# Kernel tuning notes

Hardware: AMD Instinct MI355X
Metric: run time of the kernel (lower is better)

Reference implementation:

```python
import jax, jax.numpy as jnp
import numpy as np
import math

HIDDEN = 1024
HEADS = 16
HEAD_DIM = HIDDEN // HEADS
B, S = 4, 4096


def setup_inputs() -> dict:
    key = jax.random.key(0)
    ks = jax.random.split(key, 9)
    std = 1.0 / math.sqrt(HIDDEN)
    mk = lambda k: (jax.random.normal(k, (HIDDEN, HIDDEN), jnp.float32) * std)
    return {
        "x": jax.random.normal(ks[0], (B, S, HIDDEN), jnp.float32),
        "Wq": mk(ks[1]), "bq": jnp.zeros((HIDDEN,), jnp.float32),
        "Wk": mk(ks[2]), "bk": jnp.zeros((HIDDEN,), jnp.float32),
        "Wv": mk(ks[3]), "bv": jnp.zeros((HIDDEN,), jnp.float32),
        "Wo": mk(ks[4]), "bo": jnp.zeros((HIDDEN,), jnp.float32),
    }


def reference(x, Wq, bq, Wk, bk, Wv, bv, Wo, bo):
    b, s, _ = x.shape
    scale = 1.0 / math.sqrt(HEAD_DIM)
    # projections: [b, s, hidden] -> [b, heads, s, head_dim]
    def proj(W, bias):
        y = jnp.einsum('bsh,hd->bsd', x, W.T) + bias  # torch Linear: x @ W.T + b
        return y.reshape(b, s, HEADS, HEAD_DIM).transpose(0, 2, 1, 3)
    q = proj(Wq, bq)
    k = proj(Wk, bk)
    v = proj(Wv, bv)
    # FFT along sequence axis (axis=2)
    q_f = jnp.fft.rfft(q, axis=2)
    k_f = jnp.fft.rfft(k, axis=2)
    v_f = jnp.fft.rfft(v, axis=2)
    out_f = q_f * jnp.conj(k_f) * v_f
    out = jnp.fft.irfft(out_f, n=s, axis=2) * scale
    out = out.transpose(0, 2, 1, 3).reshape(b, s, HIDDEN)
    out = jnp.einsum('bsh,hd->bsd', out, Wo.T) + bo
    # dropout is identity in eval mode
    return out
```

## Files before the change

### kernel.cpp

```cpp
#include <hip/hip_runtime.h>
#include <hip/hip_bf16.h>
#include <math.h>

#define HIDDEN   1024
#define HEADS    16
#define HEAD_DIM 64
#define BATCH    4
#define SEQ      4096
#define M_TOTAL  (BATCH * SEQ)
#define FFT_N    4096
#define WSZ      ((size_t)HIDDEN * HIDDEN)
#define PI2      6.28318530717958647692f

typedef _Float16 f16x8 __attribute__((ext_vector_type(8)));
typedef float    f32x4 __attribute__((ext_vector_type(4)));

#if defined(__has_builtin)
#if __has_builtin(__builtin_amdgcn_global_load_lds)
#define HAVE_GLL 1
#else
#define HAVE_GLL 0
#endif
#else
#define HAVE_GLL 0
#endif

#if HAVE_GLL
__device__ __forceinline__ void gload16(const void* g, void* l) {
    __builtin_amdgcn_global_load_lds(
        (const __attribute__((address_space(1))) unsigned int*)g,
        (__attribute__((address_space(3))) unsigned int*)l,
        16, 0, 0);
}
#endif

__device__ __forceinline__ void cvt8_f16(float4 v0, float4 v1,
                                         ushort* __restrict__ d) {
    const float vv[8] = {v0.x, v0.y, v0.z, v0.w, v1.x, v1.y, v1.z, v1.w};
    f16x8 hv;
    #pragma unroll
    for (int e = 0; e < 8; ++e) hv[e] = (_Float16)vv[e];
    *(f16x8*)d = hv;
}

__global__ __launch_bounds__(256) void cvt16_kernel(
    const float* __restrict__ src, ushort* __restrict__ h)
{
    const size_t i = ((size_t)blockIdx.x * 256 + threadIdx.x) * 8;
    float4 v0 = *(const float4*)(src + i);
    float4 v1 = *(const float4*)(src + i + 4);
    cvt8_f16(v0, v1, h + i);
}

__global__ __launch_bounds__(256) void cvtW_kernel(
    const float* __restrict__ Wq, const float* __restrict__ Wk,
    const float* __restrict__ Wv, const float* __restrict__ Wo,
    ushort* __restrict__ wh, ushort* __restrict__ woh)
{
    const int p = blockIdx.y;
    const size_t i = ((size_t)blockIdx.x * 256 + threadIdx.x) * 8;
    const float* __restrict__ src = (p == 0) ? Wq : (p == 1 ? Wk : (p == 2 ? Wv : Wo));
    ushort* __restrict__ dst = (p < 3) ? (wh + (size_t)p * WSZ) : woh;
    float4 v0 = *(const float4*)(src + i);
    float4 v1 = *(const float4*)(src + i + 4);
    cvt8_f16(v0, v1, dst + i);
}

__global__ __launch_bounds__(1024, 1) void gemm_qkv_mfma8(
    const ushort* __restrict__ xh, const ushort* __restrict__ wh,
    const float* __restrict__ bq, const float* __restrict__ bk,
    const float* __restrict__ bv,
    ushort* __restrict__ qkvt)
{
    __shared__ ushort Ah[3][8192];
    __shared__ ushort Bh[3][8192];

    const int tid  = threadIdx.x;
    const int lane = tid & 63;
    const int wid  = tid >> 6;
    const int wr   = wid >> 2;
    const int wc   = wid & 3;
    const int m0   = blockIdx.x * 256;
    const int ng0  = blockIdx.y * 256;
    const int p    = ng0 >> 10;
    const int n0p  = ng0 & 1023;

    const float* __restrict__ bias = (p == 0) ? bq : (p == 1 ? bk : bv);
    ushort* __restrict__ ct = qkvt + (size_t)p * HIDDEN * M_TOTAL;

    const int row = tid >> 2;
    const int chS = (tid & 3) ^ ((row >> 1) & 3);

    const int fr = lane & 15;
    const int fc = lane >> 4;
    const int cc = (fc ^ ((fr >> 1) & 3)) * 8;

    f32x4 acc[4][4];
    #pragma unroll
    for (int rf = 0; rf < 4; ++rf)
        #pragma unroll
        for (int cf = 0; cf < 4; ++cf)
            acc[rf][cf] = (f32x4){0.f, 0.f, 0.f, 0.f};

#if HAVE_GLL
    #define QKV_STAGE(K0, SLOT) {                                                  \
        const size_t gw = (size_t)(ng0 + row) * HIDDEN + (K0) + (size_t)chS * 8;   \
        const size_t gx = (size_t)(m0 + row) * HIDDEN + (K0) + (size_t)chS * 8;    \
        gload16(wh + gw, &Ah[SLOT][(size_t)tid * 8]);                              \
        gload16(xh + gx, &Bh[SLOT][(size_t)tid * 8]);                              \
    }
#else
    #define QKV_STAGE(K0, SLOT) {                                                  \
        const size_t gw = (size_t)(ng0 + row) * HIDDEN + (K0) + (size_t)chS * 8;   \
        const size_t gx = (size_t)(m0 + row) * HIDDEN + (K0) + (size_t)chS * 8;    \
        *(f16x8*)&Ah[SLOT][(size_t)tid * 8] = *(const f16x8*)(wh + gw);            \
        *(f16x8*)&Bh[SLOT][(size_t)tid * 8] = *(const f16x8*)(xh + gx);            \
    }
#endif

    QKV_STAGE(0, 0);
    QKV_STAGE(32, 1);

    for (int ks = 0; ks < 32; ++ks) {
        const int slot = ks % 3;
#if HAVE_GLL
        if (ks == 31) { asm volatile("s_waitcnt vmcnt(0)" ::: "memory"); }
        else          { asm volatile("s_waitcnt vmcnt(2)" ::: "memory"); }
        __builtin_amdgcn_s_barrier();
        asm volatile("" ::: "memory");
#else
        __syncthreads();
#endif
        {
            const ushort* pAh = Ah[slot];
            const ushort* pBh = Bh[slot];
            f16x8 a_h[4], b_h[4];
            #pragma unroll
            for (int rf = 0; rf < 4; ++rf) {
                const int R = wr * 64 + rf * 16 + fr;
                a_h[rf] = *(const f16x8*)(pAh + R * 32 + cc);
            }
            #pragma unroll
            for (int cf = 0; cf < 4; ++cf) {
                const int R = wc * 64 + cf * 16 + fr;
                b_h[cf] = *(const f16x8*)(pBh + R * 32 + cc);
            }
            #pragma unroll
            for (int rf = 0; rf < 4; ++rf)
                #pragma unroll
                for (int cf = 0; cf < 4; ++cf)
                    acc[rf][cf] = __builtin_amdgcn_mfma_f32_16x16x32_f16(a_h[rf], b_h[cf], acc[rf][cf], 0, 0, 0);
        }
        if (ks + 2 < 32) { QKV_STAGE((ks + 2) * 32, (ks + 2) % 3); }
#if !HAVE_GLL
        __syncthreads();
#endif
    }
    #undef QKV_STAGE

    const int rq = lane >> 4;
    #pragma unroll
    for (int rf = 0; rf < 4; ++rf) {
        #pragma unroll
        for (int r = 0; r < 4; ++r) {
            const int nl = wr * 64 + rf * 16 + rq * 4 + r;
            const float bv = bias[n0p + nl];
            ushort* dst = ct + (size_t)(n0p + nl) * M_TOTAL + m0 + wc * 64;
            #pragma unroll
            for (int cf = 0; cf < 4; ++cf) {
                union { _Float16 f; ushort u; } cvt;
                cvt.f = (_Float16)(acc[rf][cf][r] + bv);
                dst[cf * 16 + fr] = cvt.u;
            }
        }
    }
}

__device__ __forceinline__ float2 cmul(float2 a, float2 b) {
    return {a.x*b.x - a.y*b.y, a.x*b.y + a.y*b.x};
}

__device__ __forceinline__ int phys(int p) { return p ^ ((p >> 4) & 15); }

template<int DIR>
__device__ __forceinline__ void dft16(const float2* x, float2* X) {
    float2 t[16];
    #pragma unroll
    for (int n0 = 0; n0 < 4; ++n0) {
        float2 a = x[n0], b = x[n0+4], c = x[n0+8], d = x[n0+12];
        float2 s0 = {a.x+c.x, a.y+c.y}, s1 = {a.x-c.x, a.y-c.y};
        float2 s2 = {b.x+d.x, b.y+d.y}, s3 = {b.x-d.x, b.y-d.y};
        t[n0*4+0] = {s0.x+s2.x, s0.y+s2.y};
        t[n0*4+2] = {s0.x-s2.x, s0.y-s2.y};
        if (DIR < 0) {
            t[n0*4+1] = {s1.x+s3.y, s1.y-s3.x};
            t[n0*4+3] = {s1.x-s3.y, s1.y+s3.x};
        } else {
            t[n0*4+1] = {s1.x-s3.y, s1.y+s3.x};
            t[n0*4+3] = {s1.x+s3.y, s1.y-s3.x};
        }
    }
    const float C1 = 0.92387953251128674f;
    const float S1_ = 0.38268343236508978f;
    const float R2 = 0.70710678118654752f;
    #define TW(idx, cc_, ss_) t[idx] = cmul(t[idx], (float2){cc_, DIR*(ss_)})
    TW(1*4+1, C1, S1_);   TW(1*4+2, R2, R2);    TW(1*4+3, S1_, C1);
    TW(2*4+1, R2, R2);    TW(2*4+2, 0.f, 1.f);  TW(2*4+3, -R2, R2);
    TW(3*4+1, S1_, C1);   TW(3*4+2, -R2, R2);   TW(3*4+3, -C1, -S1_);
    #undef TW
    #pragma unroll
    for (int k0 = 0; k0 < 4; ++k0) {
        float2 a = t[0+k0], b = t[4+k0], c = t[8+k0], d = t[12+k0];
        float2 s0 = {a.x+c.x, a.y+c.y}, s1 = {a.x-c.x, a.y-c.y};
        float2 s2 = {b.x+d.x, b.y+d.y}, s3 = {b.x-d.x, b.y-d.y};
        X[k0+0]  = {s0.x+s2.x, s0.y+s2.y};
        X[k0+8]  = {s0.x-s2.x, s0.y-s2.y};
        if (DIR < 0) {
            X[k0+4]  = {s1.x+s3.y, s1.y-s3.x};
            X[k0+12] = {s1.x-s3.y, s1.y+s3.x};
        } else {
            X[k0+4]  = {s1.x-s3.y, s1.y+s3.x};
            X[k0+12] = {s1.x+s3.y, s1.y-s3.x};
        }
    }
}

__device__ __forceinline__ void twiddle_apply(float2* y, float ang) {
    float s, c;
    __sincosf(ang, &s, &c);
    const float2 base = {c, s};
    float2 w = base;
    #pragma unroll
    for (int u = 1; u < 16; ++u) {
        y[u] = cmul(y[u], w);
        w = cmul(w, base);
    }
}

__global__ __launch_bounds__(256) void fft_attn_kernel(
    const ushort* __restrict__ qt, const ushort* __restrict__ kt,
    const ushort* __restrict__ vt, float* __restrict__ ot)
{
    __shared__ float2 bufA[FFT_N];
    __shared__ float2 bufB[FFT_N];

    const int tid = threadIdx.x;
    const int bid = blockIdx.x;
    const int n   = bid >> 2;
    const int b   = bid & 3;

    const size_t off = (size_t)n * M_TOTAL + (size_t)b * SEQ;
    const _Float16* qrow = (const _Float16*)qt + off;
    const _Float16* krow = (const _Float16*)kt + off;
    const _Float16* vrow = (const _Float16*)vt + off;
    float*          orow = ot + off;

    {
        const int q = tid;
        float2 xA[16], xB[16], yA[16], yB[16];
        #pragma unroll
        for (int r = 0; r < 16; ++r) {
            xA[r] = { (float)qrow[q + 256*r], (float)krow[q + 256*r] };
            xB[r] = { (float)vrow[q + 256*r], 0.f };
        }
        dft16<-1>(xA, yA);
        dft16<-1>(xB, yB);
        const float ang = -PI2 * (float)q / 4096.f;
        twiddle_apply(yA, ang);
        twiddle_apply(yB, ang);
        #pragma unroll
        for (int u = 0; u < 16; ++u) {
            bufA[phys(q + 256*u)] = yA[u];
            bufB[phys(q + 256*u)] = yB[u];
        }
    }
    __syncthreads();
    {
        const int blk = tid >> 4, a = tid & 15;
        const int base = 256*blk + a;
        float2 xA[16], xB[16], yA[16], yB[16];
        #pragma unroll
        for (int c = 0; c < 16; ++c) {
            xA[c] = bufA[phys(base + 16*c)];
            xB[c] = bufB[phys(base + 16*c)];
        }
        dft16<-1>(xA, yA);
        dft16<-1>(xB, yB);
        const float ang = -PI2 * (float)a / 256.f;
        twiddle_apply(yA, ang);
        twiddle_apply(yB, ang);
        #pragma unroll
        for (int c = 0; c < 16; ++c) {
            bufA[phys(base + 16*c)] = yA[c];
            bufB[phys(base + 16*c)] = yB[c];
        }
    }
    __syncthreads();
    {
        const int blk = tid >> 4, c = tid & 15;
        const int base = 256*blk + 16*c;
        float2 xA[16], xB[16], yA[16], yB[16];
        #pragma unroll
        for (int a2 = 0; a2 < 16; ++a2) {
            xA[a2] = bufA[phys(base + a2)];
            xB[a2] = bufB[phys(base + a2)];
        }
        dft16<-1>(xA, yA);
        dft16<-1>(xB, yB);
        #pragma unroll
        for (int d = 0; d < 16; ++d) {
            bufA[phys(base + d)] = yA[d];
            bufB[phys(base + d)] = yB[d];
        }
    }
    __syncthreads();
    #pragma unroll
    for (int it = 0; it < 16; ++it) {
        const int p  = tid + it * 256;
        const int j  = ((p & 15) << 8) | (p & 0xF0) | (p >> 8);
        const int jn = (FFT_N - j) & (FFT_N - 1);
        const int pn = ((jn & 15) << 8) | (jn & 0xF0) | (jn >> 8);
        const float2 Zj = bufA[phys(p)];
        const float2 Zn = bufA[phys(pn)];
        const float2 Q = { 0.5f*(Zj.x + Zn.x), 0.5f*(Zj.y - Zn.y) };
        const float2 K = { 0.5f*(Zj.y + Zn.y), -0.5f*(Zj.x - Zn.x) };
        const float2 G = { Q.x*K.x + Q.y*K.y, Q.y*K.x - Q.x*K.y };
        const float2 V = bufB[phys(p)];
        bufB[phys(p)] = { G.x*V.x - G.y*V.y, G.x*V.y + G.y*V.x };
    }
    __syncthreads();
    {
        const int blk = tid >> 4, c = tid & 15;
        const int base = 256*blk + 16*c;
        float2 x[16], y[16];
        #pragma unroll
        for (int d = 0; d < 16; ++d) x[d] = bufB[phys(base + d)];
        dft16<1>(x, y);
        #pragma unroll
        for (int p0 = 0; p0 < 16; ++p0) bufB[phys(base + p0)] = y[p0];
    }
    __syncthreads();
    {
        const int blk = tid >> 4, p0 = tid & 15;
        const int base = 256*blk + p0;
        float2 x[16], y[16];
        #pragma unroll
        for (int c = 0; c < 16; ++c) x[c] = bufB[phys(base + 16*c)];
        twiddle_apply(x, PI2 * (float)p0 / 256.f);
        dft16<1>(x, y);
        #pragma unroll
        for (int p1 = 0; p1 < 16; ++p1) bufB[phys(base + 16*p1)] = y[p1];
    }
    __syncthreads();
    {
        const int qq = tid;
        float2 x[16], y[16];
        #pragma unroll
        for (int t = 0; t < 16; ++t) x[t] = bufB[phys(qq + 256*t)];
        twiddle_apply(x, PI2 * (float)qq / 4096.f);
        dft16<1>(x, y);
        const float scale = 0.125f / 4096.f;
        #pragma unroll
        for (int p2 = 0; p2 < 16; ++p2)
            orow[qq + 256*p2] = y[p2].x * scale;
    }
}

__global__ __launch_bounds__(256) void transpose_cvt_kernel(
    const float* __restrict__ ot, ushort* __restrict__ oth)
{
    __shared__ float tile[64][65];
    const int tid = threadIdx.x;
    const int m0  = blockIdx.x * 64;
    const int n0  = blockIdx.y * 64;
    const int r   = tid >> 4;
    const int c   = tid & 15;

    #pragma unroll
    for (int rr = 0; rr < 4; ++rr) {
        const int nl = r + rr * 16;
        float4 v = *(const float4*)(ot + (size_t)(n0 + nl) * M_TOTAL + m0 + c * 4);
        tile[nl][c * 4 + 0] = v.x; tile[nl][c * 4 + 1] = v.y;
        tile[nl][c * 4 + 2] = v.z; tile[nl][c * 4 + 3] = v.w;
    }
    __syncthreads();
    #pragma unroll
    for (int rr = 0; rr < 4; ++rr) {
        const int ml = r + rr * 16;
        ushort4 hh;
        union { _Float16 f; ushort u; } cv;
        cv.f = (_Float16)tile[c * 4 + 0][ml]; hh.x = cv.u;
        cv.f = (_Float16)tile[c * 4 + 1][ml]; hh.y = cv.u;
        cv.f = (_Float16)tile[c * 4 + 2][ml]; hh.z = cv.u;
        cv.f = (_Float16)tile[c * 4 + 3][ml]; hh.w = cv.u;
        *(ushort4*)(oth + (size_t)(m0 + ml) * HIDDEN + n0 + c * 4) = hh;
    }
}

__global__ __launch_bounds__(1024, 1) void gemm_out_mfma8(
    const ushort* __restrict__ oth, const ushort* __restrict__ woh,
    const float* __restrict__ bo, float* __restrict__ out)
{
    __shared__ ushort Ah[3][8192];
    __shared__ ushort Bh[3][8192];

    const int tid  = threadIdx.x;
    const int lane = tid & 63;
    const int wid  = tid >> 6;
    const int wr   = wid >> 2;
    const int wc   = wid & 3;
    const int m0   = blockIdx.x * 256;
    const int n0   = blockIdx.y * 256;

    const int row = tid >> 2;
    const int chS = (tid & 3) ^ ((row >> 1) & 3);

    const int fr = lane & 15;
    const int fc = lane >> 4;
    const int cc = (fc ^ ((fr >> 1) & 3)) * 8;

    f32x4 acc[4][4];
    #pragma unroll
    for (int rf = 0; rf < 4; ++rf)
        #pragma unroll
        for (int cf = 0; cf < 4; ++cf)
            acc[rf][cf] = (f32x4){0.f, 0.f, 0.f, 0.f};

#if HAVE_GLL
    #define OUT_STAGE(K0, SLOT) {                                                  \
        const size_t ga = (size_t)(m0 + row) * HIDDEN + (K0) + (size_t)chS * 8;    \
        const size_t gb = (size_t)(n0 + row) * HIDDEN + (K0) + (size_t)chS * 8;    \
        gload16(oth + ga, &Ah[SLOT][(size_t)tid * 8]);                             \
        gload16(woh + gb, &Bh[SLOT][(size_t)tid * 8]);                             \
    }
#else
    #define OUT_STAGE(K0, SLOT) {                                                  \
        const size_t ga = (size_t)(m0 + row) * HIDDEN + (K0) + (size_t)chS * 8;    \
        const size_t gb = (size_t)(n0 + row) * HIDDEN + (K0) + (size_t)chS * 8;    \
        *(f16x8*)&Ah[SLOT][(size_t)tid * 8] = *(const f16x8*)(oth + ga);           \
        *(f16x8*)&Bh[SLOT][(size_t)tid * 8] = *(const f16x8*)(woh + gb);           \
    }
#endif

    OUT_STAGE(0, 0);
    OUT_STAGE(32, 1);

    for (int ks = 0; ks < 32; ++ks) {
        const int slot = ks % 3;
#if HAVE_GLL
        if (ks == 31) { asm volatile("s_waitcnt vmcnt(0)" ::: "memory"); }
        else          { asm volatile("s_waitcnt vmcnt(2)" ::: "memory"); }
        __builtin_amdgcn_s_barrier();
        asm volatile("" ::: "memory");
#else
        __syncthreads();
#endif
        {
            const ushort* pAh = Ah[slot];
            const ushort* pBh = Bh[slot];
            f16x8 a_h[4], b_h[4];
            #pragma unroll
            for (int rf = 0; rf < 4; ++rf) {
                const int R = wr * 64 + rf * 16 + fr;
                a_h[rf] = *(const f16x8*)(pAh + R * 32 + cc);
            }
            #pragma unroll
            for (int cf = 0; cf < 4; ++cf) {
                const int R = wc * 64 + cf * 16 + fr;
                b_h[cf] = *(const f16x8*)(pBh + R * 32 + cc);
            }
            #pragma unroll
            for (int rf = 0; rf < 4; ++rf)
                #pragma unroll
                for (int cf = 0; cf < 4; ++cf)
                    acc[rf][cf] = __builtin_amdgcn_mfma_f32_16x16x32_f16(a_h[rf], b_h[cf], acc[rf][cf], 0, 0, 0);
        }
        if (ks + 2 < 32) { OUT_STAGE((ks + 2) * 32, (ks + 2) % 3); }
#if !HAVE_GLL
        __syncthreads();
#endif
    }
    #undef OUT_STAGE

    const int rq = lane >> 4;
    float bo_v[4];
    #pragma unroll
    for (int cf = 0; cf < 4; ++cf) bo_v[cf] = bo[n0 + wc * 64 + cf * 16 + fr];
    #pragma unroll
    for (int rf = 0; rf < 4; ++rf) {
        #pragma unroll
        for (int r = 0; r < 4; ++r) {
            const int ml = wr * 64 + rf * 16 + rq * 4 + r;
            float* dst = out + (size_t)(m0 + ml) * HIDDEN + n0 + wc * 64;
            #pragma unroll
            for (int cf = 0; cf < 4; ++cf)
                dst[cf * 16 + fr] = acc[rf][cf][r] + bo_v[cf];
        }
    }
}

extern "C" void kernel_launch(void* const* d_in, const int* in_sizes, int n_in,
                              void* d_out, int out_size, void* d_ws, size_t ws_size,
                              hipStream_t stream)
{
    const float* x  = (const float*)d_in[0];
    const float* Wq = (const float*)d_in[1];
    const float* bq = (const float*)d_in[2];
    const float* Wk = (const float*)d_in[3];
    const float* bk = (const float*)d_in[4];
    const float* Wv = (const float*)d_in[5];
    const float* bv = (const float*)d_in[6];
    const float* Wo = (const float*)d_in[7];
    const float* bo = (const float*)d_in[8];
    float* out = (float*)d_out;

    const size_t plane = (size_t)HIDDEN * M_TOTAL;
    ushort* qkvt = (ushort*)d_ws;
    ushort* qt16 = qkvt;
    ushort* kt16 = qkvt + plane;
    ushort* vt16 = qkvt + 2 * plane;
    float*  ot   = (float*)((char*)d_ws + 3 * plane * 2);
    ushort* woh  = (ushort*)((char*)d_ws + 3 * plane * 2 + plane * 4);

    ushort* oth = qkvt;

    ushort* xh  = (ushort*)d_out;
    ushort* wh  = xh + plane;

    cvt16_kernel<<<(unsigned)(plane / 2048), 256, 0, stream>>>(x, xh);
    cvtW_kernel<<<dim3((unsigned)(WSZ / 2048), 4), 256, 0, stream>>>(
        Wq, Wk, Wv, Wo, wh, woh);

    gemm_qkv_mfma8<<<dim3(M_TOTAL / 256, 12), 1024, 0, stream>>>(
        xh, wh, bq, bk, bv, qkvt);

    fft_attn_kernel<<<dim3(HIDDEN * BATCH), 256, 0, stream>>>(
        qt16, kt16, vt16, ot);

    transpose_cvt_kernel<<<dim3(M_TOTAL / 64, HIDDEN / 64), 256, 0, stream>>>(
        ot, oth);

    gemm_out_mfma8<<<dim3(M_TOTAL / 256, HIDDEN / 256), 1024, 0, stream>>>(
        oth, woh, bo, out);
}
```

Measured before the change: 276.1 us.

## Pack two batch rows per FFT block and store intermediates in fp16

The FFT attention kernel now handles two batch rows per block. It packs V of both rows into one complex FFT and Q/K of each row into separate complex FFTs, then separates the spectra by conjugate symmetry, so the inverse FFT yields both outputs as the real and imaginary parts. The Q/K spectra are kept in LDS as packed fp16 pairs to save shared memory, and the output is written as fp16 instead of fp32, which halves traffic into the transpose kernel. This cuts the FFT count per row and the memory traffic, at the cost of fp16 precision on spectral intermediates and more register pressure.

```diff
diff --git a/kernel.cpp b/kernel.cpp
--- a/kernel.cpp
+++ b/kernel.cpp
@@ -182,6 +182,16 @@
 
 __device__ __forceinline__ int phys(int p) { return p ^ ((p >> 4) & 15); }
 
+__device__ __forceinline__ unsigned pk16(float2 v) {
+    union { _Float16 f[2]; unsigned u; } c;
+    c.f[0] = (_Float16)v.x; c.f[1] = (_Float16)v.y;
+    return c.u;
+}
+__device__ __forceinline__ float2 upk16(unsigned u) {
+    union { unsigned uu; _Float16 f[2]; } c; c.uu = u;
+    return (float2){(float)c.f[0], (float)c.f[1]};
+}
+
 template<int DIR>
 __device__ __forceinline__ void dft16(const float2* x, float2* X) {
     float2 t[16];
@@ -237,101 +247,146 @@
     }
 }
 
-__global__ __launch_bounds__(256) void fft_attn_kernel(
+__global__ __launch_bounds__(256) void fft_attn_kernel2(
     const ushort* __restrict__ qt, const ushort* __restrict__ kt,
-    const ushort* __restrict__ vt, float* __restrict__ ot)
+    const ushort* __restrict__ vt, ushort* __restrict__ ot16)
 {
-    __shared__ float2 bufA[FFT_N];
+    __shared__ unsigned zA[2][FFT_N];
     __shared__ float2 bufB[FFT_N];
 
     const int tid = threadIdx.x;
     const int bid = blockIdx.x;
-    const int n   = bid >> 2;
-    const int b   = bid & 3;
-
-    const size_t off = (size_t)n * M_TOTAL + (size_t)b * SEQ;
-    const _Float16* qrow = (const _Float16*)qt + off;
-    const _Float16* krow = (const _Float16*)kt + off;
-    const _Float16* vrow = (const _Float16*)vt + off;
-    float*          orow = ot + off;
+    const int n   = bid >> 1;
+    const int bp  = bid & 1;
+
+    const size_t off0 = (size_t)n * M_TOTAL + (size_t)(2 * bp) * SEQ;
+    const size_t off1 = off0 + SEQ;
+    const _Float16* q0 = (const _Float16*)qt + off0;
+    const _Float16* k0 = (const _Float16*)kt + off0;
+    const _Float16* q1 = (const _Float16*)qt + off1;
+    const _Float16* k1 = (const _Float16*)kt + off1;
+    const _Float16* v0 = (const _Float16*)vt + off0;
+    const _Float16* v1 = (const _Float16*)vt + off1;
+    _Float16* o0 = (_Float16*)ot16 + off0;
+    _Float16* o1 = (_Float16*)ot16 + off1;
 
     {
-        const int q = tid;
-        float2 xA[16], xB[16], yA[16], yB[16];
-        #pragma unroll
-        for (int r = 0; r < 16; ++r) {
-            xA[r] = { (float)qrow[q + 256*r], (float)krow[q + 256*r] };
-            xB[r] = { (float)vrow[q + 256*r], 0.f };
-        }
-        dft16<-1>(xA, yA);
-        dft16<-1>(xB, yB);
-        const float ang = -PI2 * (float)q / 4096.f;
-        twiddle_apply(yA, ang);
-        twiddle_apply(yB, ang);
-        #pragma unroll
-        for (int u = 0; u < 16; ++u) {
-            bufA[phys(q + 256*u)] = yA[u];
-            bufB[phys(q + 256*u)] = yB[u];
+        const float ang = -PI2 * (float)tid / 4096.f;
+        {
+            float2 x[16], y[16];
+            #pragma unroll
+            for (int r = 0; r < 16; ++r)
+                x[r] = { (float)q0[tid + 256*r], (float)k0[tid + 256*r] };
+            dft16<-1>(x, y);
+            twiddle_apply(y, ang);
+            #pragma unroll
+            for (int u = 0; u < 16; ++u) zA[0][phys(tid + 256*u)] = pk16(y[u]);
+        }
+        {
+            float2 x[16], y[16];
+            #pragma unroll
+            for (int r = 0; r < 16; ++r)
+                x[r] = { (float)q1[tid + 256*r], (float)k1[tid + 256*r] };
+            dft16<-1>(x, y);
+            twiddle_apply(y, ang);
+            #pragma unroll
+            for (int u = 0; u < 16; ++u) zA[1][phys(tid + 256*u)] = pk16(y[u]);
+        }
+        {
+            float2 x[16], y[16];
+            #pragma unroll
+            for (int r = 0; r < 16; ++r)
+                x[r] = { (float)v0[tid + 256*r], (float)v1[tid + 256*r] };
+            dft16<-1>(x, y);
+            twiddle_apply(y, ang);
+            #pragma unroll
+            for (int u = 0; u < 16; ++u) bufB[phys(tid + 256*u)] = y[u];
         }
     }
     __syncthreads();
     {
         const int blk = tid >> 4, a = tid & 15;
         const int base = 256*blk + a;
-        float2 xA[16], xB[16], yA[16], yB[16];
-        #pragma unroll
-        for (int c = 0; c < 16; ++c) {
-            xA[c] = bufA[phys(base + 16*c)];
-            xB[c] = bufB[phys(base + 16*c)];
-        }
-        dft16<-1>(xA, yA);
-        dft16<-1>(xB, yB);
         const float ang = -PI2 * (float)a / 256.f;
-        twiddle_apply(yA, ang);
-        twiddle_apply(yB, ang);
-        #pragma unroll
-        for (int c = 0; c < 16; ++c) {
-            bufA[phys(base + 16*c)] = yA[c];
-            bufB[phys(base + 16*c)] = yB[c];
+        #pragma unroll
+        for (int d = 0; d < 2; ++d) {
+            float2 x[16], y[16];
+            #pragma unroll
+            for (int c = 0; c < 16; ++c) x[c] = upk16(zA[d][phys(base + 16*c)]);
+            dft16<-1>(x, y);
+            twiddle_apply(y, ang);
+            #pragma unroll
+            for (int c = 0; c < 16; ++c) zA[d][phys(base + 16*c)] = pk16(y[c]);
+        }
+        {
+            float2 x[16], y[16];
+            #pragma unroll
+            for (int c = 0; c < 16; ++c) x[c] = bufB[phys(base + 16*c)];
+            dft16<-1>(x, y);
+            twiddle_apply(y, ang);
+            #pragma unroll
+            for (int c = 0; c < 16; ++c) bufB[phys(base + 16*c)] = y[c];
         }
     }
     __syncthreads();
     {
-        const int blk = tid >> 4, c = tid & 15;
-        const int base = 256*blk + 16*c;
-        float2 xA[16], xB[16], yA[16], yB[16];
-        #pragma unroll
-        for (int a2 = 0; a2 < 16; ++a2) {
-            xA[a2] = bufA[phys(base + a2)];
-            xB[a2] = bufB[phys(base + a2)];
-        }
-        dft16<-1>(xA, yA);
-        dft16<-1>(xB, yB);
-        #pragma unroll
-        for (int d = 0; d < 16; ++d) {
-            bufA[phys(base + d)] = yA[d];
-            bufB[phys(base + d)] = yB[d];
-        }
-    }
-    __syncthreads();
+        const int base = 256*(tid >> 4) + 16*(tid & 15);
+        #pragma unroll
+        for (int d = 0; d < 2; ++d) {
+            float2 x[16], y[16];
+            #pragma unroll
+            for (int e = 0; e < 16; ++e) x[e] = upk16(zA[d][phys(base + e)]);
+            dft16<-1>(x, y);
+            #pragma unroll
+            for (int e = 0; e < 16; ++e) zA[d][phys(base + e)] = pk16(y[e]);
+        }
+        {
+            float2 x[16], y[16];
+            #pragma unroll
+            for (int e = 0; e < 16; ++e) x[e] = bufB[phys(base + e)];
+            dft16<-1>(x, y);
+            #pragma unroll
+            for (int e = 0; e < 16; ++e) bufB[phys(base + e)] = y[e];
+        }
+    }
+    __syncthreads();
+    float2 H[16];
     #pragma unroll
     for (int it = 0; it < 16; ++it) {
         const int p  = tid + it * 256;
         const int j  = ((p & 15) << 8) | (p & 0xF0) | (p >> 8);
         const int jn = (FFT_N - j) & (FFT_N - 1);
         const int pn = ((jn & 15) << 8) | (jn & 0xF0) | (jn >> 8);
-        const float2 Zj = bufA[phys(p)];
-        const float2 Zn = bufA[phys(pn)];
-        const float2 Q = { 0.5f*(Zj.x + Zn.x), 0.5f*(Zj.y - Zn.y) };
-        const float2 K = { 0.5f*(Zj.y + Zn.y), -0.5f*(Zj.x - Zn.x) };
-        const float2 G = { Q.x*K.x + Q.y*K.y, Q.y*K.x - Q.x*K.y };
-        const float2 V = bufB[phys(p)];
-        bufB[phys(p)] = { G.x*V.x - G.y*V.y, G.x*V.y + G.y*V.x };
-    }
+        const float2 Vj = bufB[phys(p)];
+        const float2 Vn = bufB[phys(pn)];
+        const float2 V1 = { 0.5f*(Vj.x + Vn.x),  0.5f*(Vj.y - Vn.y) };
+        const float2 V2 = { 0.5f*(Vj.y + Vn.y), -0.5f*(Vj.x - Vn.x) };
+        float2 F1, F2;
+        {
+            const float2 Zj = upk16(zA[0][phys(p)]);
+            const float2 Zn = upk16(zA[0][phys(pn)]);
+            const float2 Q = { 0.5f*(Zj.x + Zn.x),  0.5f*(Zj.y - Zn.y) };
+            const float2 K = { 0.5f*(Zj.y + Zn.y), -0.5f*(Zj.x - Zn.x) };
+            const float2 G = { Q.x*K.x + Q.y*K.y, Q.y*K.x - Q.x*K.y };
+            F1 = { G.x*V1.x - G.y*V1.y, G.x*V1.y + G.y*V1.x };
+        }
+        {
+            const float2 Zj = upk16(zA[1][phys(p)]);
+            const float2 Zn = upk16(zA[1][phys(pn)]);
+            const float2 Q = { 0.5f*(Zj.x + Zn.x),  0.5f*(Zj.y - Zn.y) };
+            const float2 K = { 0.5f*(Zj.y + Zn.y), -0.5f*(Zj.x - Zn.x) };
+            const float2 G = { Q.x*K.x + Q.y*K.y, Q.y*K.x - Q.x*K.y };
+            F2 = { G.x*V2.x - G.y*V2.y, G.x*V2.y + G.y*V2.x };
+        }
+        H[it] = { F1.x - F2.y, F1.y + F2.x };
+    }
+    __syncthreads();
+    #pragma unroll
+    for (int it = 0; it < 16; ++it)
+        bufB[phys(tid + it * 256)] = H[it];
     __syncthreads();
     {
-        const int blk = tid >> 4, c = tid & 15;
-        const int base = 256*blk + 16*c;
+        const int base = 256*(tid >> 4) + 16*(tid & 15);
         float2 x[16], y[16];
         #pragma unroll
         for (int d = 0; d < 16; ++d) x[d] = bufB[phys(base + d)];
@@ -361,13 +416,15 @@
         dft16<1>(x, y);
         const float scale = 0.125f / 4096.f;
         #pragma unroll
-        for (int p2 = 0; p2 < 16; ++p2)
-            orow[qq + 256*p2] = y[p2].x * scale;
+        for (int p2 = 0; p2 < 16; ++p2) {
+            o0[qq + 256*p2] = (_Float16)(y[p2].x * scale);
+            o1[qq + 256*p2] = (_Float16)(y[p2].y * scale);
+        }
     }
 }
 
 __global__ __launch_bounds__(256) void transpose_cvt_kernel(
-    const float* __restrict__ ot, ushort* __restrict__ oth)
+    const ushort* __restrict__ ot, ushort* __restrict__ oth)
 {
     __shared__ float tile[64][65];
     const int tid = threadIdx.x;
@@ -379,9 +436,12 @@
     #pragma unroll
     for (int rr = 0; rr < 4; ++rr) {
         const int nl = r + rr * 16;
-        float4 v = *(const float4*)(ot + (size_t)(n0 + nl) * M_TOTAL + m0 + c * 4);
-        tile[nl][c * 4 + 0] = v.x; tile[nl][c * 4 + 1] = v.y;
-        tile[nl][c * 4 + 2] = v.z; tile[nl][c * 4 + 3] = v.w;
+        ushort4 v = *(const ushort4*)(ot + (size_t)(n0 + nl) * M_TOTAL + m0 + c * 4);
+        union { ushort u; _Float16 f; } cv;
+        cv.u = v.x; tile[nl][c * 4 + 0] = (float)cv.f;
+        cv.u = v.y; tile[nl][c * 4 + 1] = (float)cv.f;
+        cv.u = v.z; tile[nl][c * 4 + 2] = (float)cv.f;
+        cv.u = v.w; tile[nl][c * 4 + 3] = (float)cv.f;
     }
     __syncthreads();
     #pragma unroll
@@ -519,8 +579,8 @@
     ushort* qt16 = qkvt;
     ushort* kt16 = qkvt + plane;
     ushort* vt16 = qkvt + 2 * plane;
-    float*  ot   = (float*)((char*)d_ws + 3 * plane * 2);
-    ushort* woh  = (ushort*)((char*)d_ws + 3 * plane * 2 + plane * 4);
+    ushort* ot16 = qkvt + 3 * plane;
+    ushort* woh  = ot16 + plane;
 
     ushort* oth = qkvt;
 
@@ -534,11 +594,11 @@
     gemm_qkv_mfma8<<<dim3(M_TOTAL / 256, 12), 1024, 0, stream>>>(
         xh, wh, bq, bk, bv, qkvt);
 
-    fft_attn_kernel<<<dim3(HIDDEN * BATCH), 256, 0, stream>>>(
-        qt16, kt16, vt16, ot);
+    fft_attn_kernel2<<<dim3(HIDDEN * BATCH / 2), 256, 0, stream>>>(
+        qt16, kt16, vt16, ot16);
 
     transpose_cvt_kernel<<<dim3(M_TOTAL / 64, HIDDEN / 64), 256, 0, stream>>>(
-        ot, oth);
+        ot16, oth);
 
     gemm_out_mfma8<<<dim3(M_TOTAL / 256, HIDDEN / 256), 1024, 0, stream>>>(
         oth, woh, bo, out);
```

Result: faster. 249.2 us (-9.7%).
